# Performance work log

Hardware: AMD Instinct MI355X
Metric: run time of the kernel (lower is better)

## Reference

```python
import jax, jax.numpy as jnp
import numpy as np

D_MODEL, D_STATE, D_CONV = 768, 8, 3
D_INNER = D_MODEL  # expand = 1
BATCH, SEQ = 4, 8192


def setup_inputs() -> dict:
    key = jax.random.key(0)
    ks = jax.random.split(key, 7)
    x = jax.random.normal(ks[0], (BATCH, SEQ, D_MODEL), dtype=jnp.float32)
    W_in = jax.random.normal(ks[1], (D_MODEL, 2 * D_INNER), dtype=jnp.float32) * 0.02
    conv_w = jax.random.normal(ks[2], (D_INNER, 1, D_CONV), dtype=jnp.float32) * 0.1
    conv_b = jnp.zeros((D_INNER,), dtype=jnp.float32)
    B = jax.random.normal(ks[3], (D_INNER, D_STATE), dtype=jnp.float32)
    C = jax.random.normal(ks[4], (D_INNER, D_STATE), dtype=jnp.float32)
    D = jnp.ones((D_INNER,), dtype=jnp.float32)
    W_out = jax.random.normal(ks[5], (D_INNER, D_MODEL), dtype=jnp.float32) * 0.02
    return {"x": x, "W_in": W_in, "conv_w": conv_w, "conv_b": conv_b,
            "B": B, "C": C, "D": D, "W_out": W_out}


def _forward(x, W_in, conv_w, conv_b, B, C, D, W_out):
    # in_proj and chunk
    xz = x @ W_in                                   # [B, L, 2*d_inner]
    xc, z = jnp.split(xz, 2, axis=-1)               # each [B, L, d_inner]
    # depthwise causal conv1d: torch pads (d_conv-1) both sides then slices [:L]
    # == left-pad (d_conv-1), no right pad
    xc = jnp.transpose(xc, (0, 2, 1))               # [B, d_inner, L]
    xc = jax.lax.conv_general_dilated(
        xc, conv_w,
        window_strides=(1,), padding=[(D_CONV - 1, 0)],
        dimension_numbers=("NCH", "OIH", "NCH"),
        feature_group_count=D_INNER)
    xc = xc + conv_b[None, :, None]
    xc = jnp.transpose(xc, (0, 2, 1))               # [B, L, d_inner]
    xc = jax.nn.silu(xc)
    z = jax.nn.silu(z)
    # simple SSM: h_t = h_{t-1} + outer(u_t, B); y_t = sum_s h_t*C + u_t*D
    # => y = cumsum_t(u) * sum_s(B*C) + u*D   (exact algebraic identity)
    BC = jnp.sum(B * C, axis=-1)                    # [d_inner]
    y = jnp.cumsum(xc, axis=1) * BC + xc * D
    out = (y * z) @ W_out                           # [B, L, d_model]
    return out


def reference(x, W_in, conv_w, conv_b, B, C, D, W_out):
    return _forward(x, W_in, conv_w, conv_b, B, C, D, W_out)
```

## Files before the change

### kernel.cpp

```cpp
#include <hip/hip_runtime.h>
#include <hip/hip_bf16.h>

#define D_MODEL 768
#define NSEQ    8192
#define NBATCH  4
#define MROWS   (NBATCH*NSEQ)
#define CHUNK   128
#define NCHUNK  (NSEQ/CHUNK)

typedef __attribute__((ext_vector_type(8))) short bshort8;
typedef __attribute__((ext_vector_type(4))) float f32x4;

__device__ __forceinline__ float bf2f(ushort u){
  union { unsigned int i; float f; } x; x.i = ((unsigned int)u) << 16; return x.f;
}
__device__ __forceinline__ ushort f2bf(float f){
  union { float f; unsigned int i; } x; x.f = f;
  unsigned int r = x.i + 0x7fffu + ((x.i >> 16) & 1u);
  return (ushort)(r >> 16);
}
__device__ __forceinline__ float silu_f(float v){ return v / (1.0f + __expf(-v)); }

__device__ __forceinline__ void async_copy16(const ushort* g, ushort* l){
  __builtin_amdgcn_global_load_lds((const __attribute__((address_space(1))) void*)g,
                                   (__attribute__((address_space(3))) void*)l, 16, 0, 0);
}

__global__ void tr_cvt(const float* __restrict__ in, ushort* __restrict__ out, int R, int C){
  __shared__ float tile[32][33];
  int c0 = blockIdx.x*32, r0 = blockIdx.y*32;
  int tx = threadIdx.x & 31, ty = threadIdx.x >> 5;
  #pragma unroll
  for (int p=0;p<4;p++){
    int r = ty + p*8;
    tile[r][tx] = in[(size_t)(r0+r)*C + c0 + tx];
  }
  __syncthreads();
  #pragma unroll
  for (int p=0;p<4;p++){
    int c = ty + p*8;
    out[(size_t)(c0+c)*R + r0 + tx] = f2bf(tile[tx][c]);
  }
}

__global__ void cvt_bf16(const float* __restrict__ in, ushort* __restrict__ out, int n){
  int i = (blockIdx.x*256 + threadIdx.x)*4;
  if (i >= n) return;
  const float4 f = *(const float4*)(in + i);
  ushort4 o4; o4.x=f2bf(f.x); o4.y=f2bf(f.y); o4.z=f2bf(f.z); o4.w=f2bf(f.w);
  *(ushort4*)(out + i) = o4;
}

template<int MODE>
__global__ __launch_bounds__(256) void gemm_bt(
    const ushort* __restrict__ A, const ushort* __restrict__ BT,
    ushort* __restrict__ oxc, ushort* __restrict__ oz, float* __restrict__ of,
    int K)
{
  __shared__ __align__(16) ushort Asm[128*32];
  __shared__ __align__(16) ushort Bsm[128*32];
  const int tid = threadIdx.x;
  const int bm = blockIdx.x, bn = blockIdx.y;
  const int lane = tid & 63, wid = tid >> 6;
  const int wm = (wid >> 1) * 64, wn = (wid & 1) * 64;
  const int lm = lane & 15, quad = lane >> 4;

  const ushort* Ag0 = A  + (size_t)(bm*128 +      (tid>>2))*K + (tid&3)*8;
  const ushort* Ag1 = Ag0 + (size_t)64*K;
  const ushort* Bg0 = BT + (size_t)(bn*128 +      (tid>>2))*K + (tid&3)*8;
  const ushort* Bg1 = Bg0 + (size_t)64*K;
  ushort* Al0 = Asm + tid*8;
  ushort* Al1 = Asm + 2048 + tid*8;
  ushort* Bl0 = Bsm + tid*8;
  ushort* Bl1 = Bsm + 2048 + tid*8;

  int ao[4], bo[4];
  #pragma unroll
  for (int i=0;i<4;i++){
    ao[i] = (wm + i*16 + lm)*32 + quad*8;
    bo[i] = (wn + i*16 + lm)*32 + quad*8;
  }

  f32x4 acc[4][4];
  #pragma unroll
  for (int i=0;i<4;i++)
    #pragma unroll
    for (int j=0;j<4;j++) acc[i][j] = (f32x4){0.f,0.f,0.f,0.f};

  const int KT = K >> 5;
  for (int kt=0; kt<KT; ++kt){
    __syncthreads();
    async_copy16(Ag0, Al0); async_copy16(Ag1, Al1);
    async_copy16(Bg0, Bl0); async_copy16(Bg1, Bl1);
    Ag0 += 32; Ag1 += 32; Bg0 += 32; Bg1 += 32;
    asm volatile("s_waitcnt vmcnt(0)" ::: "memory");
    __syncthreads();
    bshort8 av[4], bv[4];
    #pragma unroll
    for (int i=0;i<4;i++){
      av[i] = *(const bshort8*)(Asm + ao[i]);
      bv[i] = *(const bshort8*)(Bsm + bo[i]);
    }
    #pragma unroll
    for (int i=0;i<4;i++)
      #pragma unroll
      for (int j=0;j<4;j++)
        acc[i][j] = __builtin_amdgcn_mfma_f32_16x16x32_bf16(av[i], bv[j], acc[i][j], 0,0,0);
  }

  #pragma unroll
  for (int i=0;i<4;i++){
    int R0 = bm*128 + wm + i*16 + quad*4;
    #pragma unroll
    for (int j=0;j<4;j++){
      int Cc = bn*128 + wn + j*16 + lm;
      #pragma unroll
      for (int r=0;r<4;r++){
        int R = R0 + r;
        float v = acc[i][j][r];
        if (MODE==0){
          if (Cc < 768) oxc[(size_t)R*768 + Cc]       = f2bf(v);
          else          oz [(size_t)R*768 + (Cc-768)] = f2bf(silu_f(v));
        } else {
          of[(size_t)R*768 + Cc] = v;
        }
      }
    }
  }
}

__global__ void conv_psum(const ushort* __restrict__ xc, const float* __restrict__ cw,
                          const float* __restrict__ cb, float* __restrict__ psum){
  int c = blockIdx.y*64 + threadIdx.x;
  int b = blockIdx.z, ch = blockIdx.x;
  int t0 = ch*CHUNK;
  const ushort* xp = xc + (size_t)b*NSEQ*768 + c;
  float w0=cw[c*3+0], w1=cw[c*3+1], w2=cw[c*3+2], bb=cb[c];
  float xm2 = (t0>=2) ? bf2f(xp[(size_t)(t0-2)*768]) : 0.f;
  float xm1 = (t0>=1) ? bf2f(xp[(size_t)(t0-1)*768]) : 0.f;
  float s = 0.f;
  for (int i=0;i<CHUNK;i++){
    float x0 = bf2f(xp[(size_t)(t0+i)*768]);
    float pre = w0*xm2 + w1*xm1 + w2*x0 + bb;
    s += silu_f(pre);
    xm2 = xm1; xm1 = x0;
  }
  psum[((size_t)b*NCHUNK + ch)*768 + c] = s;
}

__global__ void scan_chunks(const float* __restrict__ psum, float* __restrict__ offs){
  int idx = blockIdx.x*256 + threadIdx.x;
  int b = idx/768, c = idx%768;
  float run = 0.f;
  for (int ch=0; ch<NCHUNK; ch++){
    size_t o = ((size_t)b*NCHUNK + ch)*768 + c;
    offs[o] = run;
    run += psum[o];
  }
}

__global__ void scan_apply(const ushort* __restrict__ xc, const ushort* __restrict__ zb,
                           const float* __restrict__ cw, const float* __restrict__ cb,
                           const float* __restrict__ Bm, const float* __restrict__ Cm,
                           const float* __restrict__ Dv, const float* __restrict__ offs,
                           ushort* __restrict__ v){
  int c = blockIdx.y*64 + threadIdx.x;
  int b = blockIdx.z, ch = blockIdx.x;
  int t0 = ch*CHUNK;
  size_t base = (size_t)b*NSEQ*768 + c;
  const ushort* xp = xc + base;
  const ushort* zp = zb + base;
  ushort* vp = v + base;
  float w0=cw[c*3+0], w1=cw[c*3+1], w2=cw[c*3+2], bb=cb[c];
  float bc = 0.f;
  #pragma unroll
  for (int s=0;s<8;s++) bc += Bm[c*8+s]*Cm[c*8+s];
  float dd = Dv[c];
  float cum = offs[((size_t)b*NCHUNK + ch)*768 + c];
  float xm2 = (t0>=2) ? bf2f(xp[(size_t)(t0-2)*768]) : 0.f;
  float xm1 = (t0>=1) ? bf2f(xp[(size_t)(t0-1)*768]) : 0.f;
  for (int i=0;i<CHUNK;i++){
    size_t o = (size_t)(t0+i)*768;
    float x0 = bf2f(xp[o]);
    float pre = w0*xm2 + w1*xm1 + w2*x0 + bb;
    float u = silu_f(pre);
    cum += u;
    float y = bc*cum + dd*u;
    vp[o] = f2bf(y * bf2f(zp[o]));
    xm2 = xm1; xm1 = x0;
  }
}

extern "C" void kernel_launch(void* const* d_in, const int* in_sizes, int n_in,
                              void* d_out, int out_size, void* d_ws, size_t ws_size,
                              hipStream_t stream)
{
  const float* x      = (const float*)d_in[0];
  const float* W_in   = (const float*)d_in[1];
  const float* conv_w = (const float*)d_in[2];
  const float* conv_b = (const float*)d_in[3];
  const float* Bm     = (const float*)d_in[4];
  const float* Cm     = (const float*)d_in[5];
  const float* Dv     = (const float*)d_in[6];
  const float* W_out  = (const float*)d_in[7];
  float* out = (float*)d_out;

  char* ws = (char*)d_ws;
  ushort* xbf   = (ushort*)(ws + 0);
  ushort* xcbf  = (ushort*)(ws + 50331648);
  ushort* zbf   = (ushort*)(ws + 100663296);
  ushort* wint  = (ushort*)(ws + 150994944);
  ushort* woutt = (ushort*)(ws + 153354240);
  float*  psum  = (float*)(ws + 154533888);
  float*  offs  = (float*)(ws + 155320320);
  if (ws_size < 156106752) return;

  tr_cvt<<<dim3(1536/32, 768/32), 256, 0, stream>>>(W_in,  wint,  768, 1536);
  tr_cvt<<<dim3(768/32,  768/32), 256, 0, stream>>>(W_out, woutt, 768, 768);
  cvt_bf16<<<(MROWS*768)/1024, 256, 0, stream>>>(x, xbf, MROWS*768);

  gemm_bt<0><<<dim3(MROWS/128, 1536/128), 256, 0, stream>>>(xbf, wint, xcbf, zbf, nullptr, 768);

  conv_psum  <<<dim3(NCHUNK, 12, NBATCH), 64, 0, stream>>>(xcbf, conv_w, conv_b, psum);
  scan_chunks<<<12, 256, 0, stream>>>(psum, offs);
  scan_apply <<<dim3(NCHUNK, 12, NBATCH), 64, 0, stream>>>(xcbf, zbf, conv_w, conv_b,
                                                           Bm, Cm, Dv, offs, xbf );

  gemm_bt<1><<<dim3(MROWS/128, 768/128), 256, 0, stream>>>(xbf, woutt, nullptr, nullptr, out, 768);
}
```

Before: 443.7 us.

## Use 32x32x16 MFMA with BK=64 and XOR-swizzled LDS tiles in GEMM

The bf16 GEMM now stages 64-wide K tiles (twice as many K elements per barrier pair) into shared memory using an XOR swizzle on 16-byte column groups to avoid LDS bank conflicts. Each wave computes its 64x64 output with four 32x32x16 MFMAs per k-step instead of sixteen 16x16x32 ones, and the epilogue is remapped to the 32x32 accumulator layout. The aim is fewer barriers and fewer LDS reads per MFMA. In exchange LDS use doubles and there is still no double buffering, so loads still do not overlap with compute.

Result: faster. 410.4 us (-7.5%).

```diff
diff --git a/kernel.cpp b/kernel.cpp
--- a/kernel.cpp
+++ b/kernel.cpp
@@ -8,8 +8,8 @@
 #define CHUNK   128
 #define NCHUNK  (NSEQ/CHUNK)
 
-typedef __attribute__((ext_vector_type(8))) short bshort8;
-typedef __attribute__((ext_vector_type(4))) float f32x4;
+typedef __attribute__((ext_vector_type(8)))  short bshort8;
+typedef __attribute__((ext_vector_type(16))) float f32x16;
 
 __device__ __forceinline__ float bf2f(ushort u){
   union { unsigned int i; float f; } x; x.i = ((unsigned int)u) << 16; return x.f;
@@ -57,67 +57,79 @@
     ushort* __restrict__ oxc, ushort* __restrict__ oz, float* __restrict__ of,
     int K)
 {
-  __shared__ __align__(16) ushort Asm[128*32];
-  __shared__ __align__(16) ushort Bsm[128*32];
+  __shared__ __align__(16) ushort Asm[128*64];
+  __shared__ __align__(16) ushort Bsm[128*64];
   const int tid = threadIdx.x;
   const int bm = blockIdx.x, bn = blockIdx.y;
   const int lane = tid & 63, wid = tid >> 6;
   const int wm = (wid >> 1) * 64, wn = (wid & 1) * 64;
-  const int lm = lane & 15, quad = lane >> 4;
-
-  const ushort* Ag0 = A  + (size_t)(bm*128 +      (tid>>2))*K + (tid&3)*8;
-  const ushort* Ag1 = Ag0 + (size_t)64*K;
-  const ushort* Bg0 = BT + (size_t)(bn*128 +      (tid>>2))*K + (tid&3)*8;
-  const ushort* Bg1 = Bg0 + (size_t)64*K;
-  ushort* Al0 = Asm + tid*8;
-  ushort* Al1 = Asm + 2048 + tid*8;
-  ushort* Bl0 = Bsm + tid*8;
-  ushort* Bl1 = Bsm + 2048 + tid*8;
-
-  int ao[4], bo[4];
-  #pragma unroll
-  for (int i=0;i<4;i++){
-    ao[i] = (wm + i*16 + lm)*32 + quad*8;
-    bo[i] = (wn + i*16 + lm)*32 + quad*8;
-  }
-
-  f32x4 acc[4][4];
-  #pragma unroll
-  for (int i=0;i<4;i++)
-    #pragma unroll
-    for (int j=0;j<4;j++) acc[i][j] = (f32x4){0.f,0.f,0.f,0.f};
-
-  const int KT = K >> 5;
+  const int l31 = lane & 31, half = lane >> 5;
+
+  const ushort* Ag[4]; const ushort* Bg[4]; ushort* Al[4]; ushort* Bl[4];
+  #pragma unroll
+  for (int it=0; it<4; ++it){
+    int p  = it*256 + tid;
+    int r  = p >> 3;
+    int cl = (p & 7) ^ (r & 7);
+    Ag[it] = A  + (size_t)(bm*128 + r)*K + cl*8;
+    Bg[it] = BT + (size_t)(bn*128 + r)*K + cl*8;
+    Al[it] = Asm + p*8;
+    Bl[it] = Bsm + p*8;
+  }
+
+  int arow[2], ar7[2], brow[2], br7[2];
+  #pragma unroll
+  for (int i=0;i<2;i++){
+    int ra = wm + i*32 + l31; arow[i] = ra*64; ar7[i] = ra & 7;
+    int rb = wn + i*32 + l31; brow[i] = rb*64; br7[i] = rb & 7;
+  }
+
+  f32x16 acc[2][2];
+  #pragma unroll
+  for (int i=0;i<2;i++)
+    #pragma unroll
+    for (int j=0;j<2;j++)
+      #pragma unroll
+      for (int r=0;r<16;r++) acc[i][j][r] = 0.f;
+
+  const int KT = K >> 6;
   for (int kt=0; kt<KT; ++kt){
     __syncthreads();
-    async_copy16(Ag0, Al0); async_copy16(Ag1, Al1);
-    async_copy16(Bg0, Bl0); async_copy16(Bg1, Bl1);
-    Ag0 += 32; Ag1 += 32; Bg0 += 32; Bg1 += 32;
+    #pragma unroll
+    for (int it=0; it<4; ++it){ async_copy16(Ag[it], Al[it]); }
+    #pragma unroll
+    for (int it=0; it<4; ++it){ async_copy16(Bg[it], Bl[it]); }
+    #pragma unroll
+    for (int it=0; it<4; ++it){ Ag[it] += 64; Bg[it] += 64; }
     asm volatile("s_waitcnt vmcnt(0)" ::: "memory");
     __syncthreads();
-    bshort8 av[4], bv[4];
-    #pragma unroll
-    for (int i=0;i<4;i++){
-      av[i] = *(const bshort8*)(Asm + ao[i]);
-      bv[i] = *(const bshort8*)(Bsm + bo[i]);
+
+    #pragma unroll
+    for (int s=0; s<4; ++s){
+      const int cbase = s*2 + half;
+      bshort8 av[2], bv[2];
+      #pragma unroll
+      for (int i=0;i<2;i++){
+        av[i] = *(const bshort8*)(Asm + arow[i] + ((cbase ^ ar7[i]) << 3));
+        bv[i] = *(const bshort8*)(Bsm + brow[i] + ((cbase ^ br7[i]) << 3));
+      }
+      acc[0][0] = __builtin_amdgcn_mfma_f32_32x32x16_bf16(av[0], bv[0], acc[0][0], 0,0,0);
+      acc[0][1] = __builtin_amdgcn_mfma_f32_32x32x16_bf16(av[0], bv[1], acc[0][1], 0,0,0);
+      acc[1][0] = __builtin_amdgcn_mfma_f32_32x32x16_bf16(av[1], bv[0], acc[1][0], 0,0,0);
+      acc[1][1] = __builtin_amdgcn_mfma_f32_32x32x16_bf16(av[1], bv[1], acc[1][1], 0,0,0);
     }
-    #pragma unroll
-    for (int i=0;i<4;i++)
+  }
+
+  #pragma unroll
+  for (int i=0;i<2;i++){
+    const int Rbase = bm*128 + wm + i*32 + 4*half;
+    #pragma unroll
+    for (int j=0;j<2;j++){
+      const int Cc = bn*128 + wn + j*32 + l31;
       #pragma unroll
-      for (int j=0;j<4;j++)
-        acc[i][j] = __builtin_amdgcn_mfma_f32_16x16x32_bf16(av[i], bv[j], acc[i][j], 0,0,0);
-  }
-
-  #pragma unroll
-  for (int i=0;i<4;i++){
-    int R0 = bm*128 + wm + i*16 + quad*4;
-    #pragma unroll
-    for (int j=0;j<4;j++){
-      int Cc = bn*128 + wn + j*16 + lm;
-      #pragma unroll
-      for (int r=0;r<4;r++){
-        int R = R0 + r;
-        float v = acc[i][j][r];
+      for (int reg=0; reg<16; reg++){
+        const int R = Rbase + (reg & 3) + 8*(reg >> 2);
+        const float v = acc[i][j][reg];
         if (MODE==0){
           if (Cc < 768) oxc[(size_t)R*768 + Cc]       = f2bf(v);
           else          oz [(size_t)R*768 + (Cc-768)] = f2bf(silu_f(v));
```
